# Kernel optimization log

Measured on AMD Instinct MI355X. Metric: run time of the kernel, lower is better.

Reference implementation:

```python
import jax, jax.numpy as jnp
import numpy as np

N_E = 1024
E_DIM = 256
BETA = 0.25
DECAY = 0.99
EPS = 1e-5


def setup_inputs() -> dict:
    key = jax.random.key(0)
    k1, k2 = jax.random.split(key)
    z = jax.random.normal(k1, (16, E_DIM, 64, 64), dtype=jnp.float32)
    # embedding.weight.data.uniform_(-1/n_e, 1/n_e)
    weight = jax.random.uniform(k2, (N_E, E_DIM), dtype=jnp.float32,
                                minval=-1.0 / N_E, maxval=1.0 / N_E)
    cluster_size = jnp.zeros((N_E,), dtype=jnp.float32)
    embedding_avg = weight  # clone of initial weight
    return {"z": z, "weight": weight, "cluster_size": cluster_size,
            "embedding_avg": embedding_avg}


def reference(z, weight, cluster_size, embedding_avg):
    B, C, H, W = z.shape  # C == e_dim
    zp = jnp.transpose(z, (0, 2, 3, 1))          # [B,H,W,C]
    zf = zp.reshape(-1, C)                       # [N, C], N = B*H*W

    # ||z||^2 + ||e||^2 - 2 z e^T  -> [N, n_e]
    d = (jnp.sum(zf * zf, axis=1, keepdims=True)
         + jnp.sum(weight * weight, axis=1)
         - 2.0 * jnp.matmul(zf, weight.T))
    idx = jnp.argmin(d, axis=1)                  # [N] int

    z_q = weight[idx].reshape(zp.shape)          # [B,H,W,C]

    # EMA codebook update (training branch), computed with scatter-sums
    n_e = weight.shape[0]
    counts = jax.ops.segment_sum(jnp.ones(zf.shape[0], dtype=zf.dtype),
                                 idx, num_segments=n_e)        # encodings.sum(0)
    new_cluster_size = cluster_size * DECAY + (1.0 - DECAY) * counts
    n = jnp.sum(new_cluster_size)
    cs_smoothed = (new_cluster_size + EPS) / (n + n_e * EPS) * n
    dw = jax.ops.segment_sum(zf, idx, num_segments=n_e)        # encodings.T @ zf
    new_embedding_avg = embedding_avg * DECAY + (1.0 - DECAY) * dw
    new_weight = new_embedding_avg / cs_smoothed[:, None]

    loss = BETA * jnp.mean((jax.lax.stop_gradient(z_q) - zp) ** 2)
    z_q_st = zp + jax.lax.stop_gradient(z_q - zp)   # straight-through
    out = jnp.transpose(z_q_st, (0, 3, 1, 2))        # back to NCHW
    return out, loss, idx, new_cluster_size, new_embedding_avg, new_weight
```

## Files before the change

kernel.cpp:

```cpp
#include <hip/hip_runtime.h>
#include <hip/hip_bf16.h>

typedef unsigned short ushort_t;
typedef __attribute__((ext_vector_type(8))) _Float16 half8;
typedef __attribute__((ext_vector_type(4))) float f32x4;

#define NB    16
#define NC    256
#define NHW   4096
#define NPIX  65536
#define NE    1024
#define BETA  0.25f
#define DECAY 0.99f
#define EPS_  1e-5f
#define GAP_FLAG 1.25e-4f

#define OFF_LOSS 16777216
#define OFF_IDXF 16777217
#define OFF_NCS  16842753
#define OFF_NEA  16843777
#define OFF_NW   17105921

#define WS_WSUM  0
#define WS_CSSM  1024
#define WS_LPART 2048
#define WS_CNT   3072
#define WS_FLAGS 3104
#define WS_LIST  5152
#define WS_WF16  40960
#define WS_ZF16  (WS_WF16 + 131072)
#define WS_END   (WS_ZF16 + 8388608)

__device__ __forceinline__ float sq_nofma(float x) {
    float s = x * x;
    asm volatile("" : "+v"(s));
    return s;
}

__device__ __forceinline__ float np_pair128_sq(const float* __restrict__ a) {
    float r[8];
    #pragma unroll
    for (int m = 0; m < 8; ++m) r[m] = sq_nofma(a[m]);
    for (int i = 8; i < 128; i += 8) {
        #pragma unroll
        for (int m = 0; m < 8; ++m) r[m] += sq_nofma(a[i + m]);
    }
    return ((r[0] + r[1]) + (r[2] + r[3])) + ((r[4] + r[5]) + (r[6] + r[7]));
}

__device__ __forceinline__ void gload16(const void* g, void* ldsp) {
    __builtin_amdgcn_global_load_lds((const __attribute__((address_space(1))) unsigned int*)g,
                                     (__attribute__((address_space(3))) unsigned int*)ldsp,
                                     16, 0, 0);
}

__global__ __launch_bounds__(256) void init_kernel(float* __restrict__ ncs,
                                                   int* __restrict__ cnt) {
    int gid = blockIdx.x * 256 + threadIdx.x;
    if (gid < NE) ncs[gid] = 0.0f;
    if (gid == 0) cnt[0] = 0;
}

__global__ __launch_bounds__(64) void wsum_kernel(const float* __restrict__ w,
                                                  float* __restrict__ wsum) {
    int j = blockIdx.x * 64 + threadIdx.x;
    const float* wr = w + (size_t)j * NC;
    wsum[j] = np_pair128_sq(wr) + np_pair128_sq(wr + 128);
}

__global__ __launch_bounds__(256) void wpack_kernel(const float* __restrict__ w,
                                                    _Float16* __restrict__ wf) {
    int i = blockIdx.x * 256 + threadIdx.x;
    wf[i] = (_Float16)(w[i] * 1024.0f);
}

__global__ __launch_bounds__(256) void zpack_kernel(const float* __restrict__ z,
                                                    _Float16* __restrict__ zf) {
    __shared__ float zs[64 * 65];
    const int t = threadIdx.x;
    const int P0 = blockIdx.x * 64;
    const int b = P0 >> 12, hw0 = P0 & (NHW - 1);
    const int K0 = blockIdx.y * 64;
    const int hw = t & 63, cq = t >> 6;
    const float* zb = z + (size_t)b * (NC * NHW) + hw0 + hw;
    #pragma unroll
    for (int i = 0; i < 16; ++i) {
        int kl = cq * 16 + i;
        zs[hw * 65 + kl] = zb[(size_t)(K0 + kl) * NHW];
    }
    __syncthreads();
    const int p = t >> 2, kq = t & 3;
    size_t obase = (size_t)(P0 + p) * NC + K0 + kq * 16;
    #pragma unroll
    for (int h2 = 0; h2 < 2; ++h2) {
        half8 v;
        #pragma unroll
        for (int j2 = 0; j2 < 8; ++j2)
            v[j2] = (_Float16)zs[p * 65 + kq * 16 + h2 * 8 + j2];
        *(half8*)&zf[obase + h2 * 8] = v;
    }
}

__global__ __launch_bounds__(256) void gemm2_kernel(const _Float16* __restrict__ wf,
                                                    const _Float16* __restrict__ zf,
                                                    const float* __restrict__ wsum,
                                                    float* __restrict__ idxf,
                                                    ushort_t* __restrict__ list,
                                                    int* __restrict__ cnt) {
    __shared__ __align__(16) _Float16 zt[128 * 256];
    __shared__ __align__(16) _Float16 wt[128 * 32];
    __shared__ float bvx[256], svx[256];
    __shared__ int   bix[256];
    __shared__ float rbv[128], rsv[128];
    __shared__ int   rbi[128];

    const int t = threadIdx.x;
    const int l = t & 63;
    const int w = t >> 6;
    const int P0 = blockIdx.x * 128;
    const int wc = w >> 1, wp = w & 1;

    #pragma unroll
    for (int i = 0; i < 16; ++i) {
        int row = w * 32 + i * 2 + (l >> 5);
        int gc = (l & 31) ^ (row & 7);
        gload16(zf + (size_t)(P0 + row) * NC + gc * 8,
                &zt[w * 8192 + i * 512 + l * 8]);
    }
    if (t < 128) { rbv[t] = 3.4e38f; rsv[t] = 3.4e38f; rbi[t] = 0; }
    __syncthreads();

    for (int ct = 0; ct < 8; ++ct) {
        f32x4 acc[4][4];
        #pragma unroll
        for (int m = 0; m < 4; ++m)
            #pragma unroll
            for (int n = 0; n < 4; ++n)
                #pragma unroll
                for (int e = 0; e < 4; ++e) acc[m][n][e] = 0.0f;

        for (int ks = 0; ks < 8; ++ks) {
            if (ks) __syncthreads();
            #pragma unroll
            for (int i = 0; i < 2; ++i) {
                int row = w * 32 + i * 16 + (l >> 2);
                int gc = (l & 3) ^ ((l >> 3) & 3);
                gload16(wf + (size_t)(ct * 128 + row) * NC + ks * 32 + gc * 8,
                        &wt[w * 1024 + i * 512 + l * 8]);
            }
            __syncthreads();

            half8 a[4], b[4];
            #pragma unroll
            for (int m = 0; m < 4; ++m) {
                int row = wc * 64 + m * 16 + (l & 15);
                int g = (l >> 4) ^ ((row >> 1) & 3);
                a[m] = *(const half8*)&wt[row * 32 + g * 8];
            }
            #pragma unroll
            for (int n = 0; n < 4; ++n) {
                int row = wp * 64 + n * 16 + (l & 15);
                int chunk = (ks * 4 + (l >> 4)) ^ (row & 7);
                b[n] = *(const half8*)&zt[row * 256 + chunk * 8];
            }
            #pragma unroll
            for (int m = 0; m < 4; ++m)
                #pragma unroll
                for (int n = 0; n < 4; ++n)
                    acc[m][n] = __builtin_amdgcn_mfma_f32_16x16x32_f16(a[m], b[n], acc[m][n], 0, 0, 0);
        }

        float en[4][4];
        #pragma unroll
        for (int m = 0; m < 4; ++m)
            #pragma unroll
            for (int r = 0; r < 4; ++r)
                en[m][r] = wsum[ct * 128 + wc * 64 + m * 16 + (l >> 4) * 4 + r];

        #pragma unroll
        for (int n = 0; n < 4; ++n) {
            float bv = 3.4e38f, sv = 3.4e38f;
            int bi = 0;
            #pragma unroll
            for (int m = 0; m < 4; ++m)
                #pragma unroll
                for (int r = 0; r < 4; ++r) {
                    float s = en[m][r] - acc[m][n][r] * 0.001953125f;
                    int code = ct * 128 + wc * 64 + m * 16 + (l >> 4) * 4 + r;
                    if (s < bv) { sv = bv; bv = s; bi = code; }
                    else if (s < sv) sv = s;
                }
            #pragma unroll
            for (int x = 16; x <= 32; x <<= 1) {
                float v2 = __shfl_xor(bv, x);
                float s2 = __shfl_xor(sv, x);
                int   i2 = __shfl_xor(bi, x);
                if (v2 < bv || (v2 == bv && i2 < bi)) { sv = fminf(bv, s2); bv = v2; bi = i2; }
                else sv = fminf(sv, v2);
            }
            if ((l >> 4) == 0) {
                int lp = wp * 64 + n * 16 + l;
                bvx[wc * 128 + lp] = bv;
                svx[wc * 128 + lp] = sv;
                bix[wc * 128 + lp] = bi;
            }
        }
        __syncthreads();
        if (t < 128) {
            float bv = bvx[t], sv = svx[t];
            int bi = bix[t];
            float v2 = bvx[128 + t], s2 = svx[128 + t];
            int i2 = bix[128 + t];
            if (v2 < bv || (v2 == bv && i2 < bi)) { sv = fminf(bv, s2); bv = v2; bi = i2; }
            else sv = fminf(sv, v2);
            if (bv < rbv[t]) { rsv[t] = fminf(rbv[t], sv); rbv[t] = bv; rbi[t] = bi; }
            else rsv[t] = fminf(rsv[t], bv);
        }
        __syncthreads();
    }

    if (t < 128) {
        int pix = P0 + t;
        idxf[pix] = (float)rbi[t];
        if (rsv[t] - rbv[t] < GAP_FLAG) {
            int pos = atomicAdd(cnt, 1);
            list[pos] = (ushort_t)pix;
        }
    }
}

__global__ __launch_bounds__(256) void argmin_kernel(const float* __restrict__ z,
                                                     const float* __restrict__ w,
                                                     const float* __restrict__ enorm,
                                                     float* __restrict__ idxf,
                                                     unsigned long long* __restrict__ flags) {
    __shared__ __align__(16) float smem[64 * 68 + 128 * 68];
    float* zt = smem;
    float* wt = smem + 64 * 68;
    const int t = threadIdx.x;
    const int pr = t & 7;
    const int cr = t >> 3;
    const int P0 = blockIdx.x * 64;
    const int b = P0 >> 12;
    const int hw0 = P0 & (NHW - 1);
    const float* zb = z + (size_t)b * (NC * NHW) + hw0;
    float bestv[8], secv[8];
    int besti[8];
    #pragma unroll
    for (int i = 0; i < 8; ++i) { bestv[i] = 3.4e38f; secv[i] = 3.4e38f; besti[i] = 0; }
    for (int cc = 0; cc < 8; ++cc) {
        float acc[8][4];
        #pragma unroll
        for (int i = 0; i < 8; ++i)
            #pragma unroll
            for (int j = 0; j < 4; ++j) acc[i][j] = 0.0f;
        for (int kc = 0; kc < 4; ++kc) {
            {
                int p = t & 63;
                int k0 = (t >> 6) * 16;
                int f2 = ((p >> 3) & 3) << 2;
                #pragma unroll
                for (int i = 0; i < 16; ++i) {
                    int k = k0 + i;
                    zt[p * 68 + (k ^ f2)] = zb[(size_t)(kc * 64 + k) * NHW + p];
                }
            }
            {
                #pragma unroll
                for (int i = 0; i < 8; ++i) {
                    int f = t + 256 * i;
                    int jj = f >> 4;
                    int k4 = f & 15;
                    float4 v = *(const float4*)&w[(size_t)(cc * 128 + jj) * NC + kc * 64 + k4 * 4];
                    *(float4*)&wt[jj * 68 + k4 * 4] = v;
                }
            }
            __syncthreads();
            #pragma unroll 2
            for (int k = 0; k < 64; k += 4) {
                float4 za[8], wb[4];
                #pragma unroll
                for (int i = 0; i < 8; ++i)
                    za[i] = *(float4*)&zt[(pr + 8 * i) * 68 + (k ^ ((i & 3) << 2))];
                #pragma unroll
                for (int j = 0; j < 4; ++j)
                    wb[j] = *(float4*)&wt[(cr + 32 * j) * 68 + k];
                #pragma unroll
                for (int i = 0; i < 8; ++i)
                    #pragma unroll
                    for (int j = 0; j < 4; ++j)
                        acc[i][j] += za[i].x * wb[j].x + za[i].y * wb[j].y +
                                     za[i].z * wb[j].z + za[i].w * wb[j].w;
            }
            __syncthreads();
        }
        #pragma unroll
        for (int j = 0; j < 4; ++j) {
            int code = cc * 128 + cr + 32 * j;
            float enj = enorm[code];
            #pragma unroll
            for (int i = 0; i < 8; ++i) {
                float s = enj - 2.0f * acc[i][j];
                if (s < bestv[i]) { secv[i] = bestv[i]; bestv[i] = s; besti[i] = code; }
                else if (s < secv[i]) secv[i] = s;
            }
        }
    }
    float* rv = smem;
    int* ri = (int*)(smem + 2048);
    float* rs = smem + 4096;
    #pragma unroll
    for (int i = 0; i < 8; ++i) {
        int p = pr + 8 * i;
        rv[p * 32 + cr] = bestv[i];
        ri[p * 32 + cr] = besti[i];
        rs[p * 32 + cr] = secv[i];
    }
    __syncthreads();
    if (t < 64) {
        int p = t;
        float bv = rv[p * 32], sv = rs[p * 32];
        int bi = ri[p * 32];
        for (int s2 = 1; s2 < 32; ++s2) {
            float v = rv[p * 32 + s2];
            float v2 = rs[p * 32 + s2];
            int ii = ri[p * 32 + s2];
            if (v < bv) { sv = bv; bv = v; bi = ii; }
            else {
                if (v < sv) sv = v;
                if (v == bv && ii < bi) bi = ii;
            }
            if (v2 < sv) sv = v2;
        }
        idxf[P0 + p] = (float)bi;
        unsigned long long mask = __ballot((sv - bv) < GAP_FLAG);
        if (t == 0) flags[blockIdx.x] = mask;
    }
}

__global__ __launch_bounds__(256) void gather_kernel(const unsigned long long* __restrict__ flags,
                                                     ushort_t* __restrict__ list,
                                                     int* __restrict__ cnt) {
    int p = blockIdx.x * 256 + threadIdx.x;
    unsigned long long m = flags[p >> 6];
    if ((m >> (p & 63)) & 1ULL) {
        int pos = atomicAdd(cnt, 1);
        list[pos] = (ushort_t)p;
    }
}

__global__ __launch_bounds__(256) void fixup3_kernel(const float* __restrict__ z,
                                                     const float* __restrict__ w,
                                                     const float* __restrict__ wsum,
                                                     const ushort_t* __restrict__ list,
                                                     const int* __restrict__ cnt,
                                                     float* __restrict__ idxf) {
    const int count = cnt[0];
    if (count == 0) return;
    const int ngroups = (count + 7) >> 3;
    const int t = threadIdx.x;

    __shared__ __align__(16) char smem_raw[16384 + 8192];
    double (*zd)[NC] = (double(*)[NC])smem_raw;
    float  (*zf)[NC] = (float(*)[NC])(smem_raw + 16384);
    float* rbv = (float*)(smem_raw + 16384);
    int*   rbi = (int*)smem_raw;
    __shared__ float zs_sh[8];
    __shared__ int   pix_sh[8];
    __shared__ float r2v[8][32];
    __shared__ int   r2i[8][32];

    for (int g = blockIdx.x; g < ngroups; g += gridDim.x) {
        if (t < 8) {
            int i = g * 8 + t;
            pix_sh[t] = (i < count) ? (int)list[i] : (int)list[0];
        }
        __syncthreads();
        #pragma unroll
        for (int px = 0; px < 8; ++px) {
            int p = pix_sh[px];
            int b = p >> 12, hw = p & (NHW - 1);
            float zv = z[(size_t)b * (NC * NHW) + (size_t)t * NHW + hw];
            zf[px][t] = zv;
            zd[px][t] = (double)zv;
        }
        __syncthreads();
        if (t < 8) zs_sh[t] = np_pair128_sq(zf[t]) + np_pair128_sq(zf[t] + 128);
        __syncthreads();

        float zs_reg[8];
        #pragma unroll
        for (int px = 0; px < 8; ++px) zs_reg[px] = zs_sh[px];

        float bvr[8];
        int   bir[8];
        #pragma unroll
        for (int px = 0; px < 8; ++px) { bvr[px] = 3.4e38f; bir[px] = 0; }

        #pragma unroll
        for (int jo = 0; jo < 2; ++jo) {
            const int j0 = t + jo * 512;
            const int j1 = j0 + 256;
            const float* wr0 = w + (size_t)j0 * NC;
            const float* wr1 = w + (size_t)j1 * NC;
            double acc0[8], acc1[8];
            #pragma unroll
            for (int px = 0; px < 8; ++px) { acc0[px] = 0.0; acc1[px] = 0.0; }
            for (int k = 0; k < NC; k += 4) {
                float4 wa = *(const float4*)&wr0[k];
                float4 wb = *(const float4*)&wr1[k];
                const float* wap = (const float*)&wa;
                const float* wbp = (const float*)&wb;
                #pragma unroll
                for (int e = 0; e < 4; ++e) {
                    double wea = (double)wap[e];
                    double web = (double)wbp[e];
                    #pragma unroll
                    for (int px = 0; px < 8; ++px) {
                        double zv = zd[px][k + e];
                        acc0[px] += wea * zv;
                        acc1[px] += web * zv;
                    }
                }
            }
            float ws0 = wsum[j0], ws1 = wsum[j1];
            #pragma unroll
            for (int px = 0; px < 8; ++px) {
                float m0 = (float)acc0[px];
                float s10 = zs_reg[px] + ws0;
                float d0 = s10 - 2.0f * m0;
                if (d0 < bvr[px] || (d0 == bvr[px] && j0 < bir[px])) { bvr[px] = d0; bir[px] = j0; }
                float m1 = (float)acc1[px];
                float s11 = zs_reg[px] + ws1;
                float d1 = s11 - 2.0f * m1;
                if (d1 < bvr[px] || (d1 == bvr[px] && j1 < bir[px])) { bvr[px] = d1; bir[px] = j1; }
            }
        }
        __syncthreads();
        #pragma unroll
        for (int px = 0; px < 8; ++px) {
            rbv[px * 256 + t] = bvr[px];
            rbi[px * 256 + t] = bir[px];
        }
        __syncthreads();
        {
            int px = t >> 5, s = t & 31;
            float bv = rbv[px * 256 + s * 8];
            int   bi = rbi[px * 256 + s * 8];
            #pragma unroll
            for (int e = 1; e < 8; ++e) {
                float v2 = rbv[px * 256 + s * 8 + e];
                int   i2 = rbi[px * 256 + s * 8 + e];
                if (v2 < bv || (v2 == bv && i2 < bi)) { bv = v2; bi = i2; }
            }
            r2v[px][s] = bv;
            r2i[px][s] = bi;
        }
        __syncthreads();
        if (t < 8) {
            float bv = r2v[t][0];
            int   bi = r2i[t][0];
            for (int s = 1; s < 32; ++s) {
                float v2 = r2v[t][s];
                int   i2 = r2i[t][s];
                if (v2 < bv || (v2 == bv && i2 < bi)) { bv = v2; bi = i2; }
            }
            if (g * 8 + t < count) idxf[pix_sh[t]] = (float)bi;
        }
        __syncthreads();
    }
}

__global__ __launch_bounds__(1024) void hist_kernel(const float* __restrict__ idxf,
                                                    float* __restrict__ ncs) {
    __shared__ int h[NE];
    int t = threadIdx.x;
    h[t] = 0;
    __syncthreads();
    int gid = blockIdx.x * 1024 + t;
    #pragma unroll
    for (int i = 0; i < 4; ++i) atomicAdd(&h[(int)idxf[gid + i * 16384]], 1);
    __syncthreads();
    if (h[t]) atomicAdd(&ncs[t], (float)h[t]);
}

__global__ __launch_bounds__(1024) void outdw_kernel(const float* __restrict__ z,
                                                     const float* __restrict__ w,
                                                     const float* __restrict__ idxf,
                                                     const float* __restrict__ ea,
                                                     float* __restrict__ outq,
                                                     float* __restrict__ nea,
                                                     float* __restrict__ lpart) {
    __shared__ float acc[NE];
    __shared__ float wcol[NE];
    __shared__ float ls[16];
    const int c = blockIdx.x;
    const int t = threadIdx.x;
    acc[t] = 0.0f;
    wcol[t] = w[(size_t)t * NC + c];
    __syncthreads();
    const float* zc = z + (size_t)c * NHW;
    float* oc = outq + (size_t)c * NHW;
    float lsum = 0.0f;
    #pragma unroll 4
    for (int i = 0; i < 16; ++i) {
        int p0 = i * 4096 + t * 4;
        size_t a = (size_t)i * (NC * NHW) + (p0 & (NHW - 1));
        float4 zv = *(const float4*)&zc[a];
        float4 iv = *(const float4*)&idxf[p0];
        int id0 = (int)iv.x, id1 = (int)iv.y, id2 = (int)iv.z, id3 = (int)iv.w;
        float4 ov;
        ov.x = wcol[id0]; ov.y = wcol[id1]; ov.z = wcol[id2]; ov.w = wcol[id3];
        *(float4*)&oc[a] = ov;
        float d0 = ov.x - zv.x, d1 = ov.y - zv.y, d2 = ov.z - zv.z, d3 = ov.w - zv.w;
        lsum += d0 * d0 + d1 * d1 + d2 * d2 + d3 * d3;
        atomicAdd(&acc[id0], zv.x);
        atomicAdd(&acc[id1], zv.y);
        atomicAdd(&acc[id2], zv.z);
        atomicAdd(&acc[id3], zv.w);
    }
    #pragma unroll
    for (int off = 32; off > 0; off >>= 1) lsum += __shfl_down(lsum, off);
    if ((t & 63) == 0) ls[t >> 6] = lsum;
    __syncthreads();
    if (t == 0) {
        float s = 0.0f;
        #pragma unroll
        for (int q = 0; q < 16; ++q) s += ls[q];
        lpart[c] = s;
    }
    size_t o = (size_t)t * NC + c;
    nea[o] = DECAY * ea[o] + (1.0f - DECAY) * acc[t];
}

__global__ __launch_bounds__(1024) void finalize_kernel(const float* __restrict__ cs,
                                                        const float* __restrict__ lpart,
                                                        float* __restrict__ ncs,
                                                        float* __restrict__ cssm,
                                                        float* __restrict__ loss) {
    int t = threadIdx.x;
    float cnt = ncs[t];
    float v = cs[t] * DECAY + (1.0f - DECAY) * cnt;
    ncs[t] = v;
    __shared__ float red[1024];
    red[t] = v;
    __syncthreads();
    for (int s = 512; s > 0; s >>= 1) {
        if (t < s) red[t] += red[t + s];
        __syncthreads();
    }
    float n = red[0];
    __syncthreads();
    cssm[t] = (v + EPS_) / (n + (float)NE * EPS_) * n;
    red[t] = (t < 256) ? lpart[t] : 0.0f;
    __syncthreads();
    for (int s = 512; s > 0; s >>= 1) {
        if (t < s) red[t] += red[t + s];
        __syncthreads();
    }
    if (t == 0) loss[0] = BETA * red[0] / 16777216.0f;
}

__global__ __launch_bounds__(256) void newweight_kernel(const float* __restrict__ nea,
                                                        const float* __restrict__ cssm,
                                                        float* __restrict__ nw) {
    int lin = blockIdx.x * 256 + threadIdx.x;
    nw[lin] = nea[lin] / cssm[lin >> 8];
}

extern "C" void kernel_launch(void* const* d_in, const int* in_sizes, int n_in,
                              void* d_out, int out_size, void* d_ws, size_t ws_size,
                              hipStream_t stream) {
    const float* z  = (const float*)d_in[0];
    const float* w  = (const float*)d_in[1];
    const float* cs = (const float*)d_in[2];
    const float* ea = (const float*)d_in[3];

    float* out  = (float*)d_out;
    float* loss = out + OFF_LOSS;
    float* idxf = out + OFF_IDXF;
    float* ncs  = out + OFF_NCS;
    float* nea  = out + OFF_NEA;
    float* nw   = out + OFF_NW;

    float* wsf = (float*)d_ws;
    float* wsum = wsf + WS_WSUM;
    float* cssm = wsf + WS_CSSM;
    float* lpart = wsf + WS_LPART;
    int* cnt = (int*)(wsf + WS_CNT);
    unsigned long long* flags = (unsigned long long*)(wsf + WS_FLAGS);
    ushort_t* list = (ushort_t*)(wsf + WS_LIST);

    hipLaunchKernelGGL(init_kernel, dim3(4), dim3(256), 0, stream, ncs, cnt);
    hipLaunchKernelGGL(wsum_kernel, dim3(16), dim3(64), 0, stream, w, wsum);

    if (ws_size >= (size_t)WS_END * 4) {
        _Float16* wf16 = (_Float16*)(wsf + WS_WF16);
        _Float16* zf16 = (_Float16*)(wsf + WS_ZF16);
        hipLaunchKernelGGL(wpack_kernel, dim3(1024), dim3(256), 0, stream, w, wf16);
        hipLaunchKernelGGL(zpack_kernel, dim3(1024, 4), dim3(256), 0, stream, z, zf16);
        hipLaunchKernelGGL(gemm2_kernel, dim3(512), dim3(256), 0, stream,
                           wf16, zf16, wsum, idxf, list, cnt);
    } else {
        hipLaunchKernelGGL(argmin_kernel, dim3(1024), dim3(256), 0, stream, z, w, wsum, idxf, flags);
        hipLaunchKernelGGL(gather_kernel, dim3(256), dim3(256), 0, stream, flags, list, cnt);
    }

    hipLaunchKernelGGL(fixup3_kernel, dim3(256), dim3(256), 0, stream, z, w, wsum, list, cnt, idxf);
    hipLaunchKernelGGL(hist_kernel, dim3(16), dim3(1024), 0, stream, idxf, ncs);
    hipLaunchKernelGGL(outdw_kernel, dim3(256), dim3(1024), 0, stream, z, w, idxf, ea, out, nea, lpart);
    hipLaunchKernelGGL(finalize_kernel, dim3(1), dim3(1024), 0, stream, cs, lpart, ncs, cssm, loss);
    hipLaunchKernelGGL(newweight_kernel, dim3(1024), dim3(256), 0, stream, nea, cssm, nw);
}
```

Measured before the change: 299.2 us.

## Split outdw across two batch halves and store int indices separately

The output/dw kernel now runs on a 256x2 grid, each half covering 8 batches. Each half writes its partial dw into the nea and nw output buffers as scratch, and a fused neaw kernel sums the two partials, applies the EMA and divides by cluster size. An int copy of the indices is written so hist and outdw skip float-to-int conversion. The intent is more parallelism in the memory-bound gather/scatter pass, at the cost of extra partial-buffer traffic and more loss partials.

```diff
diff --git a/kernel.cpp b/kernel.cpp
--- a/kernel.cpp
+++ b/kernel.cpp
@@ -29,7 +29,8 @@
 #define WS_LIST  5152
 #define WS_WF16  40960
 #define WS_ZF16  (WS_WF16 + 131072)
-#define WS_END   (WS_ZF16 + 8388608)
+#define WS_IDXI  (WS_ZF16 + 8388608)
+#define WS_END   (WS_IDXI + 65536)
 
 __device__ __forceinline__ float sq_nofma(float x) {
     float s = x * x;
@@ -105,6 +106,7 @@
                                                     const _Float16* __restrict__ zf,
                                                     const float* __restrict__ wsum,
                                                     float* __restrict__ idxf,
+                                                    int* __restrict__ idxi,
                                                     ushort_t* __restrict__ list,
                                                     int* __restrict__ cnt) {
     __shared__ __align__(16) _Float16 zt[128 * 256];
@@ -222,6 +224,7 @@
     if (t < 128) {
         int pix = P0 + t;
         idxf[pix] = (float)rbi[t];
+        idxi[pix] = rbi[t];
         if (rsv[t] - rbv[t] < GAP_FLAG) {
             int pos = atomicAdd(cnt, 1);
             list[pos] = (ushort_t)pix;
@@ -233,6 +236,7 @@
                                                      const float* __restrict__ w,
                                                      const float* __restrict__ enorm,
                                                      float* __restrict__ idxf,
+                                                     int* __restrict__ idxi,
                                                      unsigned long long* __restrict__ flags) {
     __shared__ __align__(16) float smem[64 * 68 + 128 * 68];
     float* zt = smem;
@@ -333,6 +337,7 @@
             if (v2 < sv) sv = v2;
         }
         idxf[P0 + p] = (float)bi;
+        idxi[P0 + p] = bi;
         unsigned long long mask = __ballot((sv - bv) < GAP_FLAG);
         if (t == 0) flags[blockIdx.x] = mask;
     }
@@ -354,7 +359,8 @@
                                                      const float* __restrict__ wsum,
                                                      const ushort_t* __restrict__ list,
                                                      const int* __restrict__ cnt,
-                                                     float* __restrict__ idxf) {
+                                                     float* __restrict__ idxf,
+                                                     int* __restrict__ idxi) {
     const int count = cnt[0];
     if (count == 0) return;
     const int ngroups = (count + 7) >> 3;
@@ -465,13 +471,16 @@
                 int   i2 = r2i[t][s];
                 if (v2 < bv || (v2 == bv && i2 < bi)) { bv = v2; bi = i2; }
             }
-            if (g * 8 + t < count) idxf[pix_sh[t]] = (float)bi;
-        }
-        __syncthreads();
-    }
-}
-
-__global__ __launch_bounds__(1024) void hist_kernel(const float* __restrict__ idxf,
+            if (g * 8 + t < count) {
+                idxf[pix_sh[t]] = (float)bi;
+                idxi[pix_sh[t]] = bi;
+            }
+        }
+        __syncthreads();
+    }
+}
+
+__global__ __launch_bounds__(1024) void hist_kernel(const int* __restrict__ idxi,
                                                     float* __restrict__ ncs) {
     __shared__ int h[NE];
     int t = threadIdx.x;
@@ -479,22 +488,23 @@
     __syncthreads();
     int gid = blockIdx.x * 1024 + t;
     #pragma unroll
-    for (int i = 0; i < 4; ++i) atomicAdd(&h[(int)idxf[gid + i * 16384]], 1);
+    for (int i = 0; i < 4; ++i) atomicAdd(&h[idxi[gid + i * 16384]], 1);
     __syncthreads();
     if (h[t]) atomicAdd(&ncs[t], (float)h[t]);
 }
 
 __global__ __launch_bounds__(1024) void outdw_kernel(const float* __restrict__ z,
                                                      const float* __restrict__ w,
-                                                     const float* __restrict__ idxf,
-                                                     const float* __restrict__ ea,
+                                                     const int* __restrict__ idxi,
                                                      float* __restrict__ outq,
-                                                     float* __restrict__ nea,
+                                                     float* __restrict__ dw0,
+                                                     float* __restrict__ dw1,
                                                      float* __restrict__ lpart) {
     __shared__ float acc[NE];
     __shared__ float wcol[NE];
     __shared__ float ls[16];
     const int c = blockIdx.x;
+    const int part = blockIdx.y;
     const int t = threadIdx.x;
     acc[t] = 0.0f;
     wcol[t] = w[(size_t)t * NC + c];
@@ -502,22 +512,22 @@
     const float* zc = z + (size_t)c * NHW;
     float* oc = outq + (size_t)c * NHW;
     float lsum = 0.0f;
-    #pragma unroll 4
-    for (int i = 0; i < 16; ++i) {
-        int p0 = i * 4096 + t * 4;
-        size_t a = (size_t)i * (NC * NHW) + (p0 & (NHW - 1));
+    #pragma unroll
+    for (int i = 0; i < 8; ++i) {
+        int b = part * 8 + i;
+        int p0 = b * 4096 + t * 4;
+        size_t a = (size_t)b * (NC * NHW) + t * 4;
         float4 zv = *(const float4*)&zc[a];
-        float4 iv = *(const float4*)&idxf[p0];
-        int id0 = (int)iv.x, id1 = (int)iv.y, id2 = (int)iv.z, id3 = (int)iv.w;
+        int4 iv = *(const int4*)&idxi[p0];
         float4 ov;
-        ov.x = wcol[id0]; ov.y = wcol[id1]; ov.z = wcol[id2]; ov.w = wcol[id3];
+        ov.x = wcol[iv.x]; ov.y = wcol[iv.y]; ov.z = wcol[iv.z]; ov.w = wcol[iv.w];
         *(float4*)&oc[a] = ov;
         float d0 = ov.x - zv.x, d1 = ov.y - zv.y, d2 = ov.z - zv.z, d3 = ov.w - zv.w;
         lsum += d0 * d0 + d1 * d1 + d2 * d2 + d3 * d3;
-        atomicAdd(&acc[id0], zv.x);
-        atomicAdd(&acc[id1], zv.y);
-        atomicAdd(&acc[id2], zv.z);
-        atomicAdd(&acc[id3], zv.w);
+        atomicAdd(&acc[iv.x], zv.x);
+        atomicAdd(&acc[iv.y], zv.y);
+        atomicAdd(&acc[iv.z], zv.z);
+        atomicAdd(&acc[iv.w], zv.w);
     }
     #pragma unroll
     for (int off = 32; off > 0; off >>= 1) lsum += __shfl_down(lsum, off);
@@ -527,10 +537,10 @@
         float s = 0.0f;
         #pragma unroll
         for (int q = 0; q < 16; ++q) s += ls[q];
-        lpart[c] = s;
-    }
-    size_t o = (size_t)t * NC + c;
-    nea[o] = DECAY * ea[o] + (1.0f - DECAY) * acc[t];
+        lpart[c * 2 + part] = s;
+    }
+    float* dwp = part ? dw1 : dw0;
+    dwp[(size_t)t * NC + c] = acc[t];
 }
 
 __global__ __launch_bounds__(1024) void finalize_kernel(const float* __restrict__ cs,
@@ -552,7 +562,7 @@
     float n = red[0];
     __syncthreads();
     cssm[t] = (v + EPS_) / (n + (float)NE * EPS_) * n;
-    red[t] = (t < 256) ? lpart[t] : 0.0f;
+    red[t] = (t < 512) ? lpart[t] : 0.0f;
     __syncthreads();
     for (int s = 512; s > 0; s >>= 1) {
         if (t < s) red[t] += red[t + s];
@@ -561,11 +571,15 @@
     if (t == 0) loss[0] = BETA * red[0] / 16777216.0f;
 }
 
-__global__ __launch_bounds__(256) void newweight_kernel(const float* __restrict__ nea,
-                                                        const float* __restrict__ cssm,
-                                                        float* __restrict__ nw) {
+__global__ __launch_bounds__(256) void neaw_kernel(const float* __restrict__ ea,
+                                                   const float* __restrict__ cssm,
+                                                   float* __restrict__ nea,
+                                                   float* __restrict__ nw) {
     int lin = blockIdx.x * 256 + threadIdx.x;
-    nw[lin] = nea[lin] / cssm[lin >> 8];
+    float dw = nea[lin] + nw[lin];
+    float v = DECAY * ea[lin] + (1.0f - DECAY) * dw;
+    nea[lin] = v;
+    nw[lin] = v / cssm[lin >> 8];
 }
 
 extern "C" void kernel_launch(void* const* d_in, const int* in_sizes, int n_in,
@@ -590,6 +604,7 @@
     int* cnt = (int*)(wsf + WS_CNT);
     unsigned long long* flags = (unsigned long long*)(wsf + WS_FLAGS);
     ushort_t* list = (ushort_t*)(wsf + WS_LIST);
+    int* idxi = (int*)(wsf + WS_IDXI);
 
     hipLaunchKernelGGL(init_kernel, dim3(4), dim3(256), 0, stream, ncs, cnt);
     hipLaunchKernelGGL(wsum_kernel, dim3(16), dim3(64), 0, stream, w, wsum);
@@ -600,15 +615,15 @@
         hipLaunchKernelGGL(wpack_kernel, dim3(1024), dim3(256), 0, stream, w, wf16);
         hipLaunchKernelGGL(zpack_kernel, dim3(1024, 4), dim3(256), 0, stream, z, zf16);
         hipLaunchKernelGGL(gemm2_kernel, dim3(512), dim3(256), 0, stream,
-                           wf16, zf16, wsum, idxf, list, cnt);
+                           wf16, zf16, wsum, idxf, idxi, list, cnt);
     } else {
-        hipLaunchKernelGGL(argmin_kernel, dim3(1024), dim3(256), 0, stream, z, w, wsum, idxf, flags);
+        hipLaunchKernelGGL(argmin_kernel, dim3(1024), dim3(256), 0, stream, z, w, wsum, idxf, idxi, flags);
         hipLaunchKernelGGL(gather_kernel, dim3(256), dim3(256), 0, stream, flags, list, cnt);
     }
 
-    hipLaunchKernelGGL(fixup3_kernel, dim3(256), dim3(256), 0, stream, z, w, wsum, list, cnt, idxf);
-    hipLaunchKernelGGL(hist_kernel, dim3(16), dim3(1024), 0, stream, idxf, ncs);
-    hipLaunchKernelGGL(outdw_kernel, dim3(256), dim3(1024), 0, stream, z, w, idxf, ea, out, nea, lpart);
+    hipLaunchKernelGGL(fixup3_kernel, dim3(256), dim3(256), 0, stream, z, w, wsum, list, cnt, idxf, idxi);
+    hipLaunchKernelGGL(hist_kernel, dim3(16), dim3(1024), 0, stream, idxi, ncs);
+    hipLaunchKernelGGL(outdw_kernel, dim3(256, 2), dim3(1024), 0, stream, z, w, idxi, out, nea, nw, lpart);
     hipLaunchKernelGGL(finalize_kernel, dim3(1), dim3(1024), 0, stream, cs, lpart, ncs, cssm, loss);
-    hipLaunchKernelGGL(newweight_kernel, dim3(1024), dim3(256), 0, stream, nea, cssm, nw);
-}
+    hipLaunchKernelGGL(neaw_kernel, dim3(1024), dim3(256), 0, stream, ea, cssm, nea, nw);
+}
```

Measured after the change: 299.0 us. No clear change (-0.1%).
